# Kernel tuning notes

Measured on AMD Instinct MI355X. Metric: run time of the kernel, lower is better.

## Reference

```python
import jax, jax.numpy as jnp
import numpy as np

N = 50000      # nodes
E = 800000     # edges
D_IN = 128
D_H = 128
D_OUT = 64


def _glorot(key, fan_in, fan_out):
    s = float(np.sqrt(6.0 / (fan_in + fan_out)))
    return jax.random.uniform(key, (fan_in, fan_out), jnp.float32, -s, s)


def setup_inputs() -> dict:
    key = jax.random.key(0)
    ks = jax.random.split(key, 8)
    x = jax.random.normal(ks[0], (N, D_IN), jnp.float32)
    edge_index = jax.random.randint(ks[1], (2, E), 0, N, dtype=jnp.int32)
    return {
        "x": x,
        "edge_index": edge_index,
        "W0": _glorot(ks[2], D_IN, D_H), "b0": jnp.zeros((D_H,), jnp.float32),
        "W1": _glorot(ks[3], D_H, D_H),  "b1": jnp.zeros((D_H,), jnp.float32),
        "W2": _glorot(ks[4], D_H, D_H),  "b2": jnp.zeros((D_H,), jnp.float32),
        "W_out": _glorot(ks[5], D_H, D_OUT), "b_out": jnp.zeros((D_OUT,), jnp.float32),
    }


def reference(x, edge_index, W0, b0, W1, b1, W2, b2, W_out, b_out):
    src = edge_index[0]
    dst = edge_index[1]
    # GCN normalization with self-loops: deg = in-degree(dst) + 1
    deg = jax.ops.segment_sum(jnp.ones((E,), x.dtype), dst, num_segments=N) + 1.0
    dinv = jax.lax.rsqrt(deg)                       # [N]
    edge_coef = (dinv[src] * dinv[dst])[:, None]    # [E,1]
    self_coef = (dinv * dinv)[:, None]              # [N,1]

    def gcn_conv(h, W, b):
        h = h @ W                                            # [N,F]
        agg = jax.ops.segment_sum(h[src] * edge_coef, dst, num_segments=N)
        agg = agg + h * self_coef                            # self-loop term
        return agg + b

    h = x
    for W, b in ((W0, b0), (W1, b1), (W2, b2)):
        h_in = h
        h = jax.nn.relu(gcn_conv(h, W, b))  # eval mode: dropout is identity
        if h.shape == h_in.shape:
            h = h + h_in
    return h @ W_out + b_out
```

## Files before the change

### kernel.cpp

```cpp
#include <hip/hip_runtime.h>

#define N_NODES 50000
#define N_EDGES 800000
#define NB512 98

static inline int cdiv(int a, int b) { return (a + b - 1) / b; }

typedef __attribute__((ext_vector_type(8))) short s8vec;
typedef __attribute__((ext_vector_type(4))) float f32x4;

__device__ inline ushort f2b(float f) {
    uint u = __float_as_uint(f);
    uint r = (u + 0x7fffu + ((u >> 16) & 1u)) >> 16;
    return (ushort)r;
}
__device__ inline float b2f_lo(uint v) { return __uint_as_float(v << 16); }
__device__ inline float b2f_hi(uint v) { return __uint_as_float(v & 0xffff0000u); }

__device__ inline void add8(float* acc, uint4 v) {
    acc[0] += b2f_lo(v.x); acc[1] += b2f_hi(v.x);
    acc[2] += b2f_lo(v.y); acc[3] += b2f_hi(v.y);
    acc[4] += b2f_lo(v.z); acc[5] += b2f_hi(v.z);
    acc[6] += b2f_lo(v.w); acc[7] += b2f_hi(v.w);
}


__global__ __launch_bounds__(256) void k_prep(int* cnt,
                                              const float* __restrict__ W0, const float* __restrict__ W1,
                                              const float* __restrict__ W2, const float* __restrict__ Wo,
                                              ushort* Wt0, ushort* Wt1, ushort* Wt2, ushort* Wto) {
    int b = blockIdx.x;
    if (b < 196) {
        int i = b * 256 + threadIdx.x;
        if (i < N_NODES) cnt[i] = 0;
        return;
    }
    int i = (b - 196) * 256 + threadIdx.x;
    if (i < 16384) {
        int nn = i >> 7, k = i & 127;
        Wt0[i] = f2b(W0[k * 128 + nn]);
    } else if (i < 32768) {
        int j = i - 16384; int nn = j >> 7, k = j & 127;
        Wt1[j] = f2b(W1[k * 128 + nn]);
    } else if (i < 49152) {
        int j = i - 32768; int nn = j >> 7, k = j & 127;
        Wt2[j] = f2b(W2[k * 128 + nn]);
    } else if (i < 57344) {
        int j = i - 49152; int nn = j >> 7, k = j & 127;
        Wto[j] = f2b(Wo[k * 64 + nn]);
    }
}

__global__ __launch_bounds__(256) void k_count(const int* __restrict__ dst, int* cnt, int e) {
    int i = blockIdx.x * 256 + threadIdx.x;
    if (i < e) atomicAdd(&cnt[dst[i]], 1);
}


__global__ __launch_bounds__(512) void k_scan_all(const int* __restrict__ cnt,
                                                  int* rowptr, int* cursor, float* dinv,
                                                  int n, int e, int nb) {
    __shared__ int sh[512];
    int t = threadIdx.x, b = blockIdx.x;
    int start = b * 512;

    int partial = 0;
    for (int i = t; i < start; i += 512) partial += cnt[i];
    sh[t] = partial;
    __syncthreads();
    for (int off = 256; off > 0; off >>= 1) {
        if (t < off) sh[t] += sh[t + off];
        __syncthreads();
    }
    int base = sh[0];
    __syncthreads();

    int i = start + t;
    int v = (i < n) ? cnt[i] : 0;
    sh[t] = v;
    __syncthreads();
    for (int off = 1; off < 512; off <<= 1) {
        int add = (t >= off) ? sh[t - off] : 0;
        __syncthreads();
        sh[t] += add;
        __syncthreads();
    }
    if (i < n) {
        int rp = base + sh[t] - v;
        rowptr[i] = rp;
        cursor[i] = rp;
        dinv[i] = rsqrtf((float)v + 1.0f);
    }
    if (b == nb - 1 && t == 0) rowptr[n] = e;
}


template <int NCOL, bool IN_F32, bool OUT_F32, bool SCALE>
__device__ inline void mm_body(const void* __restrict__ Av, const ushort* __restrict__ Wt,
                               const float* __restrict__ bias, const float* __restrict__ dinv,
                               void* __restrict__ Cv, int n, int bid) {
    constexpr int NT = NCOL / 16;
    int wave = threadIdx.x >> 6;
    int lane = threadIdx.x & 63;
    int quad = lane >> 4;
    int lm = lane & 15;
    int row0 = bid * 128 + wave * 32;

    int rA0 = row0 + lm;      if (rA0 > n - 1) rA0 = n - 1;
    int rA1 = row0 + 16 + lm; if (rA1 > n - 1) rA1 = n - 1;

    f32x4 acc[2][NT];
#pragma unroll
    for (int r = 0; r < 2; r++)
#pragma unroll
        for (int t = 0; t < NT; t++) acc[r][t] = (f32x4){0.f, 0.f, 0.f, 0.f};

    for (int kc = 0; kc < 128; kc += 32) {
        s8vec af[2];
        if (IN_F32) {
            const float* A = (const float*)Av;
#pragma unroll
            for (int r = 0; r < 2; r++) {
                const float* p = A + (size_t)(r ? rA1 : rA0) * 128 + quad * 8 + kc;
                float4 a = *(const float4*)p, b = *(const float4*)(p + 4);
                s8vec v;
                v[0] = (short)f2b(a.x); v[1] = (short)f2b(a.y);
                v[2] = (short)f2b(a.z); v[3] = (short)f2b(a.w);
                v[4] = (short)f2b(b.x); v[5] = (short)f2b(b.y);
                v[6] = (short)f2b(b.z); v[7] = (short)f2b(b.w);
                af[r] = v;
            }
        } else {
            const ushort* A = (const ushort*)Av;
            af[0] = *(const s8vec*)(A + (size_t)rA0 * 128 + quad * 8 + kc);
            af[1] = *(const s8vec*)(A + (size_t)rA1 * 128 + quad * 8 + kc);
        }
#pragma unroll
        for (int t = 0; t < NT; t++) {
            s8vec bf = *(const s8vec*)(Wt + (size_t)(t * 16 + lm) * 128 + kc + quad * 8);
            acc[0][t] = __builtin_amdgcn_mfma_f32_16x16x32_bf16(af[0], bf, acc[0][t], 0, 0, 0);
            acc[1][t] = __builtin_amdgcn_mfma_f32_16x16x32_bf16(af[1], bf, acc[1][t], 0, 0, 0);
        }
    }

#pragma unroll
    for (int r = 0; r < 2; r++) {
#pragma unroll
        for (int i = 0; i < 4; i++) {
            int rr = row0 + r * 16 + quad * 4 + i;
            if (rr < n) {
                float dv = SCALE ? dinv[rr] : 1.0f;
#pragma unroll
                for (int t = 0; t < NT; t++) {
                    int col = t * 16 + lm;
                    if (OUT_F32)
                        ((float*)Cv)[(size_t)rr * NCOL + col] = acc[r][t][i] + bias[col];
                    else
                        ((ushort*)Cv)[(size_t)rr * 128 + col] =
                            f2b(SCALE ? acc[r][t][i] * dv : acc[r][t][i]);
                }
            }
        }
    }
}

__global__ __launch_bounds__(256) void k_mm0_fill(const void* __restrict__ Av,
                                                  const ushort* __restrict__ Wt,
                                                  const float* __restrict__ dinv,
                                                  void* __restrict__ Cv, int n, int mmblocks,
                                                  const int* __restrict__ src, const int* __restrict__ dst,
                                                  int* cursor, uint* ed, int e) {
    if ((int)blockIdx.x >= mmblocks) {
        int base = ((int)blockIdx.x - mmblocks) * 1024 + threadIdx.x;
#pragma unroll
        for (int k = 0; k < 4; k++) {
            int i = base + k * 256;
            if (i < e) {
                int d = dst[i], s = src[i];
                int pos = atomicAdd(&cursor[d], 1);
                ed[pos] = (uint)s;
            }
        }
        return;
    }
    mm_body<128, true, false, true>(Av, Wt, nullptr, dinv, Cv, n, blockIdx.x);
}


template <int NCOL, bool RES_F32, bool FINAL>
__global__ __launch_bounds__(256) void k_gather_mm(const uint4* __restrict__ T4,
                                                   const int* __restrict__ rowptr,
                                                   const uint* __restrict__ ed,
                                                   const float* __restrict__ dinv,
                                                   const float* __restrict__ biasL,
                                                   const void* __restrict__ resv,
                                                   uint4* __restrict__ hout,
                                                   const ushort* __restrict__ Wt,
                                                   const float* __restrict__ bias_out,
                                                   void* __restrict__ Cv, int n) {
    __shared__ uint4 As4[16 * 17];
    ushort* As = (ushort*)As4;

    int tid = threadIdx.x;
    int nl = tid >> 4, ql = tid & 15;
    int qb = tid & 48;
    int node = blockIdx.x * 16 + nl;

    float acc[8] = {0.f, 0.f, 0.f, 0.f, 0.f, 0.f, 0.f, 0.f};
    int beg = rowptr[node], end = rowptr[node + 1];

    for (int base = beg; base < end; base += 16) {
        int m = end - base; if (m > 16) m = 16;
        int idx = base + ql; if (idx > end - 1) idx = end - 1;
        uint em = ed[idx];
        int j = 0;
        for (; j + 4 <= m; j += 4) {
            int s0 = __shfl((int)em, qb + j);
            int s1 = __shfl((int)em, qb + j + 1);
            int s2 = __shfl((int)em, qb + j + 2);
            int s3 = __shfl((int)em, qb + j + 3);
            uint4 v0 = T4[(size_t)s0 * 16 + ql];
            uint4 v1 = T4[(size_t)s1 * 16 + ql];
            uint4 v2 = T4[(size_t)s2 * 16 + ql];
            uint4 v3 = T4[(size_t)s3 * 16 + ql];
            add8(acc, v0); add8(acc, v1); add8(acc, v2); add8(acc, v3);
        }
        for (; j < m; j++) {
            int s = __shfl((int)em, qb + j);
            uint4 v = T4[(size_t)s * 16 + ql];
            add8(acc, v);
        }
    }

    uint4 vs = T4[(size_t)node * 16 + ql];
    add8(acc, vs);

    float di = dinv[node];
    float4 bv0 = ((const float4*)biasL)[ql * 2];
    float4 bv1 = ((const float4*)biasL)[ql * 2 + 1];
    float bb[8] = {bv0.x, bv0.y, bv0.z, bv0.w, bv1.x, bv1.y, bv1.z, bv1.w};

    float r[8];
    if (RES_F32) {
        float4 r0 = ((const float4*)resv)[(size_t)node * 32 + ql * 2];
        float4 r1 = ((const float4*)resv)[(size_t)node * 32 + ql * 2 + 1];
        r[0] = r0.x; r[1] = r0.y; r[2] = r0.z; r[3] = r0.w;
        r[4] = r1.x; r[5] = r1.y; r[6] = r1.z; r[7] = r1.w;
    } else {
        uint4 rv = ((const uint4*)resv)[(size_t)node * 16 + ql];
        r[0] = b2f_lo(rv.x); r[1] = b2f_hi(rv.x); r[2] = b2f_lo(rv.y); r[3] = b2f_hi(rv.y);
        r[4] = b2f_lo(rv.z); r[5] = b2f_hi(rv.z); r[6] = b2f_lo(rv.w); r[7] = b2f_hi(rv.w);
    }

    float o[8];
#pragma unroll
    for (int i = 0; i < 8; i++)
        o[i] = fmaxf(acc[i] * di + bb[i], 0.f) + r[i];

    uint4 ov;
    ov.x = (uint)f2b(o[0]) | ((uint)f2b(o[1]) << 16);
    ov.y = (uint)f2b(o[2]) | ((uint)f2b(o[3]) << 16);
    ov.z = (uint)f2b(o[4]) | ((uint)f2b(o[5]) << 16);
    ov.w = (uint)f2b(o[6]) | ((uint)f2b(o[7]) << 16);

    if (!FINAL) hout[(size_t)node * 16 + ql] = ov;
    *(uint4*)&As[nl * 136 + ql * 8] = ov;
    __syncthreads();

    constexpr int NT = NCOL / 64;
    int wave = tid >> 6;
    int lane = tid & 63;
    int quad = lane >> 4;
    int lm = lane & 15;

    f32x4 macc[NT];
#pragma unroll
    for (int t = 0; t < NT; t++) macc[t] = (f32x4){0.f, 0.f, 0.f, 0.f};

    for (int kc = 0; kc < 128; kc += 32) {
        s8vec af = *(const s8vec*)&As[lm * 136 + kc + quad * 8];
#pragma unroll
        for (int t = 0; t < NT; t++) {
            int col = wave * (16 * NT) + t * 16 + lm;
            s8vec bf = *(const s8vec*)(Wt + (size_t)col * 128 + kc + quad * 8);
            macc[t] = __builtin_amdgcn_mfma_f32_16x16x32_bf16(af, bf, macc[t], 0, 0, 0);
        }
    }

    int row0 = blockIdx.x * 16;
#pragma unroll
    for (int t = 0; t < NT; t++) {
        int col = wave * (16 * NT) + t * 16 + lm;
#pragma unroll
        for (int i = 0; i < 4; i++) {
            int rr = row0 + quad * 4 + i;
            if (FINAL)
                ((float*)Cv)[(size_t)rr * 64 + col] = macc[t][i] + bias_out[col];
            else
                ((ushort*)Cv)[(size_t)rr * 128 + col] = f2b(macc[t][i] * dinv[rr]);
        }
    }
}


extern "C" void kernel_launch(void* const* d_in, const int* in_sizes, int n_in,
                              void* d_out, int out_size, void* d_ws, size_t ws_size,
                              hipStream_t stream) {
    const float* x  = (const float*)d_in[0];
    const int* eidx = (const int*)d_in[1];
    const float* W0 = (const float*)d_in[2];
    const float* b0 = (const float*)d_in[3];
    const float* W1 = (const float*)d_in[4];
    const float* b1 = (const float*)d_in[5];
    const float* W2 = (const float*)d_in[6];
    const float* b2 = (const float*)d_in[7];
    const float* Wo = (const float*)d_in[8];
    const float* bo = (const float*)d_in[9];
    float* out = (float*)d_out;

    const int N = N_NODES, E = N_EDGES;
    const int* srcI = eidx;
    const int* dstI = eidx + E;

    char* ws = (char*)d_ws;
    auto alloc = [&](size_t bytes) { char* p = ws; ws += (bytes + 255) / 256 * 256; return p; };
    int*    cnt    = (int*)alloc((size_t)N * 4);
    int*    cursor = (int*)alloc((size_t)N * 4);
    int*    rowptr = (int*)alloc((size_t)(N + 1) * 4);
    float*  dinv   = (float*)alloc((size_t)N * 4);
    uint*   ed     = (uint*)alloc((size_t)E * 4);
    ushort* tA     = (ushort*)alloc((size_t)N * 128 * 2);
    ushort* tB     = (ushort*)alloc((size_t)N * 128 * 2);
    ushort* hAb    = (ushort*)alloc((size_t)N * 128 * 2);
    ushort* hBb    = (ushort*)alloc((size_t)N * 128 * 2);
    ushort* Wt0    = (ushort*)alloc(128 * 128 * 2);
    ushort* Wt1    = (ushort*)alloc(128 * 128 * 2);
    ushort* Wt2    = (ushort*)alloc(128 * 128 * 2);
    ushort* Wto    = (ushort*)alloc(64 * 128 * 2);

    dim3 b256(256), b512(512);

    const int mmGrid   = cdiv(N, 128);
    const int fillGrid = cdiv(E, 1024);
    const int gGrid    = N / 16;

    k_prep<<<196 + 224, b256, 0, stream>>>(cnt, W0, W1, W2, Wo, Wt0, Wt1, Wt2, Wto);
    k_count<<<cdiv(E, 256), b256, 0, stream>>>(dstI, cnt, E);
    k_scan_all<<<NB512, b512, 0, stream>>>(cnt, rowptr, cursor, dinv, N, E, NB512);

    k_mm0_fill<<<mmGrid + fillGrid, b256, 0, stream>>>(x, Wt0, dinv, tA, N, mmGrid,
                                                       srcI, dstI, cursor, ed, E);

    k_gather_mm<128, true, false><<<gGrid, b256, 0, stream>>>(
        (const uint4*)tA, rowptr, ed, dinv, b0, x, (uint4*)hAb, Wt1, nullptr, tB, N);

    k_gather_mm<128, false, false><<<gGrid, b256, 0, stream>>>(
        (const uint4*)tB, rowptr, ed, dinv, b1, hAb, (uint4*)hBb, Wt2, nullptr, tA, N);

    k_gather_mm<64, false, true><<<gGrid, b256, 0, stream>>>(
        (const uint4*)tA, rowptr, ed, dinv, b2, hBb, nullptr, Wto, bo, out, N);
}
```

Before: 299.8 us.

## Record per-edge rank in count pass and store edge sources as 16-bit

The counting kernel now saves the value returned by its atomic increment as a per-edge rank. The fill step can then place each edge at rowptr[dst] + rank with a plain store, instead of doing a second atomic on a cursor array, and the cursor array is removed. The CSR source list is also narrowed from 32-bit to 16-bit indices, which halves the index traffic in each of the three gather kernels. The cost is an extra 4-byte-per-edge rank array that is written and read once, and the 16-bit indices only work because the node count stays below 65536.

```diff
diff --git a/kernel.cpp b/kernel.cpp
--- a/kernel.cpp
+++ b/kernel.cpp
@@ -51,14 +51,15 @@
     }
 }
 
-__global__ __launch_bounds__(256) void k_count(const int* __restrict__ dst, int* cnt, int e) {
+__global__ __launch_bounds__(256) void k_count(const int* __restrict__ dst, int* cnt,
+                                               int* __restrict__ rank, int e) {
     int i = blockIdx.x * 256 + threadIdx.x;
-    if (i < e) atomicAdd(&cnt[dst[i]], 1);
+    if (i < e) rank[i] = atomicAdd(&cnt[dst[i]], 1);
 }
 
 
 __global__ __launch_bounds__(512) void k_scan_all(const int* __restrict__ cnt,
-                                                  int* rowptr, int* cursor, float* dinv,
+                                                  int* rowptr, float* dinv,
                                                   int n, int e, int nb) {
     __shared__ int sh[512];
     int t = threadIdx.x, b = blockIdx.x;
@@ -86,9 +87,7 @@
         __syncthreads();
     }
     if (i < n) {
-        int rp = base + sh[t] - v;
-        rowptr[i] = rp;
-        cursor[i] = rp;
+        rowptr[i] = base + sh[t] - v;
         dinv[i] = rsqrtf((float)v + 1.0f);
     }
     if (b == nb - 1 && t == 0) rowptr[n] = e;
@@ -169,16 +168,18 @@
                                                   const float* __restrict__ dinv,
                                                   void* __restrict__ Cv, int n, int mmblocks,
                                                   const int* __restrict__ src, const int* __restrict__ dst,
-                                                  int* cursor, uint* ed, int e) {
+                                                  const int* __restrict__ rank,
+                                                  const int* __restrict__ rowptr,
+                                                  ushort* ed, int e) {
     if ((int)blockIdx.x >= mmblocks) {
         int base = ((int)blockIdx.x - mmblocks) * 1024 + threadIdx.x;
 #pragma unroll
         for (int k = 0; k < 4; k++) {
             int i = base + k * 256;
             if (i < e) {
-                int d = dst[i], s = src[i];
-                int pos = atomicAdd(&cursor[d], 1);
-                ed[pos] = (uint)s;
+                int d = dst[i];
+                int pos = rowptr[d] + rank[i];
+                ed[pos] = (ushort)src[i];
             }
         }
         return;
@@ -190,7 +191,7 @@
 template <int NCOL, bool RES_F32, bool FINAL>
 __global__ __launch_bounds__(256) void k_gather_mm(const uint4* __restrict__ T4,
                                                    const int* __restrict__ rowptr,
-                                                   const uint* __restrict__ ed,
+                                                   const ushort* __restrict__ ed,
                                                    const float* __restrict__ dinv,
                                                    const float* __restrict__ biasL,
                                                    const void* __restrict__ resv,
@@ -325,10 +326,10 @@
     char* ws = (char*)d_ws;
     auto alloc = [&](size_t bytes) { char* p = ws; ws += (bytes + 255) / 256 * 256; return p; };
     int*    cnt    = (int*)alloc((size_t)N * 4);
-    int*    cursor = (int*)alloc((size_t)N * 4);
     int*    rowptr = (int*)alloc((size_t)(N + 1) * 4);
+    int*    rank   = (int*)alloc((size_t)E * 4);
     float*  dinv   = (float*)alloc((size_t)N * 4);
-    uint*   ed     = (uint*)alloc((size_t)E * 4);
+    ushort* ed     = (ushort*)alloc((size_t)E * 2);
     ushort* tA     = (ushort*)alloc((size_t)N * 128 * 2);
     ushort* tB     = (ushort*)alloc((size_t)N * 128 * 2);
     ushort* hAb    = (ushort*)alloc((size_t)N * 128 * 2);
@@ -345,11 +346,11 @@
     const int gGrid    = N / 16;
 
     k_prep<<<196 + 224, b256, 0, stream>>>(cnt, W0, W1, W2, Wo, Wt0, Wt1, Wt2, Wto);
-    k_count<<<cdiv(E, 256), b256, 0, stream>>>(dstI, cnt, E);
-    k_scan_all<<<NB512, b512, 0, stream>>>(cnt, rowptr, cursor, dinv, N, E, NB512);
+    k_count<<<cdiv(E, 256), b256, 0, stream>>>(dstI, cnt, rank, E);
+    k_scan_all<<<NB512, b512, 0, stream>>>(cnt, rowptr, dinv, N, E, NB512);
 
     k_mm0_fill<<<mmGrid + fillGrid, b256, 0, stream>>>(x, Wt0, dinv, tA, N, mmGrid,
-                                                       srcI, dstI, cursor, ed, E);
+                                                       srcI, dstI, rank, rowptr, ed, E);
 
     k_gather_mm<128, true, false><<<gGrid, b256, 0, stream>>>(
         (const uint4*)tA, rowptr, ed, dinv, b0, x, (uint4*)hAb, Wt1, nullptr, tB, N);
```

Result: faster. 276.2 us (-7.9%).
